# Kernel optimization log

Hardware: AMD Instinct MI355X
Metric: run time of the kernel (lower is better)

The kernel has to match this reference:

```python
import jax, jax.numpy as jnp
import numpy as np

B, S = 256, 512
NQ = 1000           # n_skills
MEM, DK, DV, FC = 20, 50, 200, 50  # memory_size, key dim, value dim, final fc dim


def _kaiming(key, shape, fan_in):
    return jax.random.normal(key, shape) * np.float32(np.sqrt(2.0 / fan_in))


def setup_inputs() -> dict:
    key = jax.random.key(0)
    ks = jax.random.split(key, 12)
    q_data = jax.random.randint(ks[0], (B, S), 0, NQ + 1)
    qa_data = jax.random.randint(ks[1], (B, S), 0, 2 * NQ + 1)
    u = jax.random.uniform(ks[2], (B * S,))
    # target: -1 = masked/padding, else binary label (matches target.ge(0) masking)
    target = jnp.where(u < 0.1, -1.0, (u > 0.55).astype(jnp.float32))
    q_embed_w = _kaiming(ks[3], (NQ + 1, DK), DK)
    qa_embed_w = _kaiming(ks[4], (2 * NQ + 1, DV), DV)
    memory_key = _kaiming(ks[5], (MEM, DK), DK)
    init_memory_value = _kaiming(ks[6], (MEM, DV), DV)
    erase_w = _kaiming(ks[7], (DV, DV), DV)
    erase_b = jnp.zeros((DV,), jnp.float32)
    add_w = _kaiming(ks[8], (DV, DV), DV)
    add_b = jnp.zeros((DV,), jnp.float32)
    read_w = _kaiming(ks[9], (DV + FC, FC), DV + FC)
    read_b = jnp.zeros((FC,), jnp.float32)
    pred_w = _kaiming(ks[10], (FC, 1), FC)
    pred_b = jnp.zeros((1,), jnp.float32)
    return dict(q_data=q_data, qa_data=qa_data, target=target,
                q_embed_w=q_embed_w, qa_embed_w=qa_embed_w,
                memory_key=memory_key, init_memory_value=init_memory_value,
                erase_w=erase_w, erase_b=erase_b, add_w=add_w, add_b=add_b,
                read_w=read_w, read_b=read_b, pred_w=pred_w, pred_b=pred_b)


def reference(q_data, qa_data, target, q_embed_w, qa_embed_w, memory_key,
              init_memory_value, erase_w, erase_b, add_w, add_b,
              read_w, read_b, pred_w, pred_b):
    b = q_data.shape[0]
    q_e = q_embed_w[q_data]     # [B,S,DK]
    qa_e = qa_embed_w[qa_data]  # [B,S,DV]
    Mv0 = jnp.broadcast_to(init_memory_value, (b, MEM, DV))

    def step(Mv, xs):
        q_t, qa_t = xs                                        # [B,DK], [B,DV]
        corr = jax.nn.softmax(q_t @ memory_key.T, axis=1)     # [B,MEM] addressing
        read = jnp.einsum('bm,bmd->bd', corr, Mv)             # weighted read
        erase = jax.nn.sigmoid(qa_t @ erase_w + erase_b)      # [B,DV]
        add = jnp.tanh(qa_t @ add_w + add_b)                  # [B,DV]
        w = corr[:, :, None]                                  # [B,MEM,1]
        Mv = Mv * (1.0 - w * erase[:, None, :]) + w * add[:, None, :]
        return Mv, read

    _, reads = jax.lax.scan(step, Mv0, (q_e.transpose(1, 0, 2), qa_e.transpose(1, 0, 2)))
    reads = reads.transpose(1, 0, 2)                          # [B,S,DV]
    x = jnp.concatenate([reads, q_e], axis=-1)                # [B,S,DV+FC]
    h = jnp.tanh(x @ read_w + read_b)                         # [B,S,FC]
    logits = (h @ pred_w + pred_b).reshape(-1)                # [B*S]
    mask = target >= 0.0
    t = jnp.where(mask, target, 0.0)
    # numerically-stable BCE-with-logits, masked mean
    bce = jnp.maximum(logits, 0.0) - logits * t + jnp.log1p(jnp.exp(-jnp.abs(logits)))
    loss = jnp.sum(jnp.where(mask, bce, 0.0)) / jnp.maximum(mask.sum(), 1)
    return loss, jax.nn.sigmoid(logits)
```

## Files before the change

### kernel.cpp

```cpp
#include <hip/hip_runtime.h>
#include <math.h>

#define B_   256
#define S_   512
#define NQ_  1000
#define MEM_ 20
#define DK_  50
#define DV_  200
#define FC_  50
#define RPB  2
#define CHK  16
#define CLEN (S_/CHK)
#define NKS  7
#define XS_STRIDE 232
#define CORR_STRIDE 12
#define NB_EA    ((2*NQ_+1+RPB-1)/RPB)
#define NB_CORR  4
#define NB_WPACK 7
#define NB_HQ    251
#define PREP1_BLOCKS (NB_EA+NB_CORR)
#define MM_BLOCKS (B_*CHK)
#define SCANA_BLOCKS (B_*(CHK-1))
#define SCANA_TOTAL (SCANA_BLOCKS+NB_WPACK+NB_HQ)

typedef __attribute__((ext_vector_type(8))) short bf16x8_t;
typedef __attribute__((ext_vector_type(4))) float f32x4_t;
typedef __attribute__((ext_vector_type(2))) _Float16 f16x2_t;

static __device__ __forceinline__ f16x2_t h2(unsigned u){ return __builtin_bit_cast(f16x2_t, u); }
static __device__ __forceinline__ unsigned h2u(f16x2_t v){ return __builtin_bit_cast(unsigned, v); }
static __device__ __forceinline__ unsigned packh2(float x, float y){
  unsigned short bx = __builtin_bit_cast(unsigned short, (_Float16)x);
  unsigned short by = __builtin_bit_cast(unsigned short, (_Float16)y);
  return (unsigned)bx | ((unsigned)by << 16);
}
static __device__ __forceinline__ f16x2_t pkfma16(f16x2_t a, f16x2_t b, f16x2_t c){
  return __builtin_elementwise_fma(a, b, c);
}
static __device__ __forceinline__ f16x2_t splat_l(f16x2_t p){ return __builtin_shufflevector(p, p, 0, 0); }
static __device__ __forceinline__ f16x2_t splat_h(f16x2_t p){ return __builtin_shufflevector(p, p, 1, 1); }

static __device__ __forceinline__ unsigned short f2bf(float f){
  unsigned u = __float_as_uint(f);
  unsigned r = u + 0x7fffu + ((u >> 16) & 1u);
  return (unsigned short)(r >> 16);
}
static __device__ __forceinline__ float ftanh(float x){
  float e = __expf(2.f*x);
  return 1.f - 2.f*__builtin_amdgcn_rcpf(e+1.f);
}
static __device__ __forceinline__ float fsigm(float x){
  return __builtin_amdgcn_rcpf(1.f+__expf(-x));
}

__global__ __launch_bounds__(256) void k_prep1(
    const float* __restrict__ qaw,
    const float* __restrict__ ew, const float* __restrict__ eb,
    const float* __restrict__ aw, const float* __restrict__ ab,
    unsigned* __restrict__ eaTab,
    const float* __restrict__ qw, const float* __restrict__ mk,
    unsigned* __restrict__ corrH){
  __shared__ float qa[RPB*DV_];
  int blk = blockIdx.x;
  if(blk < NB_EA){
    int row0 = blk*RPB;
    for(int i=threadIdx.x; i<RPB*DV_; i+=256){
      int r = i/DV_, cc = i - r*DV_;
      int row = row0 + r;
      qa[i] = (row <= 2*NQ_) ? qaw[row*DV_+cc] : 0.f;
    }
    __syncthreads();
    int d = threadIdx.x;
    if(d >= DV_) return;
    float accE[RPB], accA[RPB];
    #pragma unroll
    for(int r=0;r<RPB;++r){ accE[r] = eb[d]; accA[r] = ab[d]; }
    float we0 = ew[d], wa0 = aw[d];
    for(int j=0;j<DV_;++j){
      int jn = (j+1 < DV_) ? j+1 : j;
      float we1 = ew[jn*DV_+d];
      float wa1 = aw[jn*DV_+d];
      #pragma unroll
      for(int r=0;r<RPB;++r){
        float x = qa[r*DV_+j];
        accE[r] = fmaf(x, we0, accE[r]);
        accA[r] = fmaf(x, wa0, accA[r]);
      }
      we0 = we1; wa0 = wa1;
    }
    #pragma unroll
    for(int r=0;r<RPB;++r){
      int row = row0 + r;
      if(row <= 2*NQ_){
        unsigned he = (unsigned)__builtin_bit_cast(unsigned short, (_Float16)fsigm(accE[r]));
        unsigned ha = (unsigned)__builtin_bit_cast(unsigned short, (_Float16)ftanh(accA[r]));
        eaTab[(size_t)row*DV_+d] = he | (ha << 16);
      }
    }
  } else {
    int q = (blk-NB_EA)*256 + threadIdx.x;
    if(q > NQ_) return;
    float qv[DK_];
    #pragma unroll
    for(int j=0;j<DK_;++j) qv[j] = qw[q*DK_+j];
    float s[MEM_]; float mx = -1e30f;
    #pragma unroll
    for(int m=0;m<MEM_;++m){
      float acc = 0.f;
      #pragma unroll
      for(int j=0;j<DK_;++j) acc = fmaf(qv[j], mk[m*DK_+j], acc);
      s[m] = acc; mx = fmaxf(mx, acc);
    }
    float sum = 0.f;
    #pragma unroll
    for(int m=0;m<MEM_;++m){ s[m] = __expf(s[m]-mx); sum += s[m]; }
    float inv = __builtin_amdgcn_rcpf(sum);
    #pragma unroll
    for(int i=0;i<MEM_/2;++i)
      corrH[q*CORR_STRIDE+i] = packh2(s[2*i]*inv, s[2*i+1]*inv);
  }
}

#define STAGE_CHUNK(QP_G, QAP_G) { \
  int td = threadIdx.x; \
  if(td < CLEN){ \
    eaOffL[td] = (unsigned)(QAP_G)[td] * (DV_*4u); \
  } else if(td >= 64 && td < 64+160){ \
    int k = td - 64; \
    int t_ = (k*13108) >> 16;    \
    int j_ = k - t_*5; \
    int row_ = (QP_G)[t_]; \
    *(uint2*)&crL[t_*12 + j_*2] = \
      *(const uint2*)(corrH + (size_t)row_*CORR_STRIDE + j_*2); \
  } }

__global__ __launch_bounds__(256,8) void k_scanA(const int* __restrict__ qd,
    const int* __restrict__ qad,
    const unsigned* __restrict__ corrH,
    const unsigned* __restrict__ eaTab,
    unsigned* __restrict__ ABu,
    const float* __restrict__ qw,
    const float* __restrict__ rw, const float* __restrict__ rb,
    const float* __restrict__ pw,
    unsigned short* __restrict__ WpFrag, float* __restrict__ pwPad,
    float* __restrict__ hq){
  __shared__ __align__(16) unsigned crL[CLEN*12];
  __shared__ unsigned eaOffL[CLEN];
  const int blk = blockIdx.x;
  if(blk >= SCANA_BLOCKS){
    int xblk = blk - SCANA_BLOCKS;
    if(xblk < NB_WPACK){
      int ks = xblk;
      int nt = threadIdx.x >> 6;
      int lane = threadIdx.x & 63;
      int quad = lane >> 4, col = lane & 15;
      int n = nt*16 + col;
      unsigned short tmp[8];
      #pragma unroll
      for(int j=0;j<8;++j){
        int k = ks*32 + quad*8 + j;
        tmp[j] = (k < DV_ && n < FC_) ? f2bf(rw[k*FC_+n]) : (unsigned short)0;
      }
      uint4* dst = reinterpret_cast<uint4*>(WpFrag + ((size_t)(ks*4+nt)*64 + lane)*8);
      *dst = *reinterpret_cast<const uint4*>(tmp);
      if(ks == 0 && threadIdx.x < 64)
        pwPad[threadIdx.x] = (threadIdx.x < FC_) ? pw[threadIdx.x] : 0.f;
    } else {
      int idx = (xblk-NB_WPACK)*256 + threadIdx.x;
      int q = idx >> 6, n = idx & 63;
      if(q > NQ_) return;
      float v = 0.f;
      if(n < FC_){
        float acc = rb[n];
        #pragma unroll
        for(int j=0;j<DK_;++j)
          acc = fmaf(qw[q*DK_+j], rw[(DV_+j)*FC_+n], acc);
        v = acc;
      }
      hq[q*64+n] = v;
    }
    return;
  }

  const int b = blk / (CHK-1), c = blk % (CHK-1);
  const int d = threadIdx.x;
  const int dc = (d < DV_) ? d : DV_-1;
  const bool act = (d < DV_);
  const int* __restrict__ qp  = qd  + b*S_ + c*CLEN;
  const int* __restrict__ qap = qad + b*S_ + c*CLEN;

  STAGE_CHUNK(qp, qap)

  const f16x2_t one2h = {(_Float16)1.f, (_Float16)1.f};
  f16x2_t A2[MEM_/2], B2[MEM_/2];
  #pragma unroll
  for(int i=0;i<MEM_/2;++i){ A2[i] = one2h; B2[i] = (f16x2_t){(_Float16)0.f,(_Float16)0.f}; }

  __syncthreads();

  const char* eaB = (const char*)eaTab;
  const unsigned dcB = (unsigned)dc*4u;
  unsigned ea0 = *(const unsigned*)(eaB + eaOffL[0] + dcB);
  unsigned ea1 = *(const unsigned*)(eaB + eaOffL[1] + dcB);
  unsigned ea2 = *(const unsigned*)(eaB + eaOffL[2] + dcB);
  unsigned off3 = eaOffL[3], off4 = eaOffL[4], off5 = eaOffL[5];
  uint4 ca0 = *(const uint4*)&crL[0];  uint4 cb0 = *(const uint4*)&crL[4];  uint2 cc0 = *(const uint2*)&crL[8];
  uint4 ca1 = *(const uint4*)&crL[12]; uint4 cb1 = *(const uint4*)&crL[16]; uint2 cc1 = *(const uint2*)&crL[20];

  #pragma unroll 4
  for(int t=0;t<CLEN;++t){
    int t2 = (t+2 < CLEN) ? t+2 : CLEN-1;
    uint4 ca2 = *(const uint4*)&crL[t2*12];
    uint4 cb2 = *(const uint4*)&crL[t2*12+4];
    uint2 cc2 = *(const uint2*)&crL[t2*12+8];
    unsigned eanew = *(const unsigned*)(eaB + off3 + dcB);
    int t6 = (t+6 < CLEN) ? t+6 : CLEN-1;
    unsigned offnew = eaOffL[t6];

    f16x2_t pe = h2(ea0);
    const f16x2_t ee = splat_l(pe), aa = splat_h(pe);
    #define UPDA(u, i) { \
      f16x2_t cp = h2(u); \
      f16x2_t al = pkfma16(-cp, ee, one2h); \
      f16x2_t be = cp*aa; \
      A2[i] = A2[i]*al; \
      B2[i] = pkfma16(al, B2[i], be); }
    UPDA(ca0.x, 0)  UPDA(ca0.y, 1)  UPDA(ca0.z, 2)  UPDA(ca0.w, 3)
    UPDA(cb0.x, 4)  UPDA(cb0.y, 5)  UPDA(cb0.z, 6)  UPDA(cb0.w, 7)
    UPDA(cc0.x, 8)  UPDA(cc0.y, 9)
    #undef UPDA

    ca0=ca1; cb0=cb1; cc0=cc1;
    ca1=ca2; cb1=cb2; cc1=cc2;
    ea0=ea1; ea1=ea2; ea2=eanew;
    off3=off4; off4=off5; off5=offnew;
  }
  if(act){
    unsigned* base = ABu + ((size_t)(b*(CHK-1) + c)*MEM_)*DV_ + d;
    #pragma unroll
    for(int i=0;i<MEM_/2;++i){
      unsigned a01 = h2u(A2[i]);
      unsigned b01 = h2u(B2[i]);
      base[(size_t)(2*i)*DV_]   = (a01 & 0xffffu) | (b01 << 16);
      base[(size_t)(2*i+1)*DV_] = (a01 >> 16)     | (b01 & 0xffff0000u);
    }
  }
}

__global__ __launch_bounds__(256) void k_prefix(const float* __restrict__ mv0,
    const unsigned* __restrict__ ABu, unsigned* __restrict__ Mv0p){
  int i = blockIdx.x*256 + threadIdx.x;
  if(i >= B_*(MEM_/2)*DV_) return;
  int d = i % DV_;
  int p = (i / DV_) % (MEM_/2);
  int b = i / (DV_*(MEM_/2));
  float MvE = mv0[(2*p)*DV_+d];
  float MvO = mv0[(2*p+1)*DV_+d];
  #pragma unroll
  for(int c=1;c<CHK;++c){
    unsigned vE = ABu[((size_t)(b*(CHK-1) + (c-1))*MEM_ + 2*p)*DV_ + d];
    unsigned vO = ABu[((size_t)(b*(CHK-1) + (c-1))*MEM_ + 2*p+1)*DV_ + d];
    MvE = fmaf((float)h2(vE)[0], MvE, (float)h2(vE)[1]);
    MvO = fmaf((float)h2(vO)[0], MvO, (float)h2(vO)[1]);
    Mv0p[((size_t)(b*CHK + c)*(MEM_/2) + p)*DV_ + d] = packh2(MvE, MvO);
  }
}

__global__ __launch_bounds__(256,8) void k_scan_mm(const int* __restrict__ qd,
    const int* __restrict__ qad,
    const unsigned* __restrict__ corrH,
    const unsigned* __restrict__ eaTab,
    const float* __restrict__ mv0,
    const unsigned* __restrict__ Mv0p,
    const unsigned short* __restrict__ WpFrag,
    const float* __restrict__ hq,
    const float* __restrict__ pwPad, const float* __restrict__ pb,
    const float* __restrict__ target,
    float* __restrict__ out, float2* __restrict__ partials){
  __shared__ unsigned short Xs[CLEN*XS_STRIDE];
  __shared__ __align__(16) unsigned crL[CLEN*12];
  __shared__ unsigned eaOffL[CLEN];
  __shared__ float sred[2][2][16];
  __shared__ float sbce[4];

  const int blk = blockIdx.x;
  const int b = blk >> 4, c = blk & (CHK-1);
  const int d = threadIdx.x;
  const int dc = (d < DV_) ? d : DV_-1;
  const bool act = (d < DV_);
  const bool padw = (d < 224);
  const int* __restrict__ qp  = qd  + b*S_ + c*CLEN;
  const int* __restrict__ qap = qad + b*S_ + c*CLEN;

  const int wave = threadIdx.x >> 6;
  const int lane = threadIdx.x & 63;
  const int col  = lane & 15, quad = lane >> 4;
  const int rt   = wave & 1;
  const int nh   = wave >> 1;
  const int mbase = rt*16;

  STAGE_CHUNK(qp, qap)

  int qpre[4];
  #pragma unroll
  for(int reg=0;reg<4;++reg) qpre[reg] = qp[mbase + quad*4 + reg];

  f16x2_t Mv2[MEM_/2];
  if(c == 0){
    #pragma unroll
    for(int i=0;i<MEM_/2;++i)
      Mv2[i] = (f16x2_t){ (_Float16)mv0[(2*i)*DV_+dc], (_Float16)mv0[(2*i+1)*DV_+dc] };
  } else {
    const unsigned* base = Mv0p + ((size_t)(b*CHK + c)*(MEM_/2))*DV_ + dc;
    #pragma unroll
    for(int i=0;i<MEM_/2;++i)
      Mv2[i] = h2(base[(size_t)i*DV_]);
  }

  __syncthreads();

  const char* eaB = (const char*)eaTab;
  const unsigned dcB = (unsigned)dc*4u;
  unsigned ea0 = *(const unsigned*)(eaB + eaOffL[0] + dcB);
  unsigned ea1 = *(const unsigned*)(eaB + eaOffL[1] + dcB);
  unsigned ea2 = *(const unsigned*)(eaB + eaOffL[2] + dcB);
  unsigned off3 = eaOffL[3], off4 = eaOffL[4], off5 = eaOffL[5];
  uint4 ca0 = *(const uint4*)&crL[0];  uint4 cb0 = *(const uint4*)&crL[4];  uint2 cc0 = *(const uint2*)&crL[8];
  uint4 ca1 = *(const uint4*)&crL[12]; uint4 cb1 = *(const uint4*)&crL[16]; uint2 cc1 = *(const uint2*)&crL[20];

  #pragma unroll 4
  for(int t=0;t<CLEN;++t){
    int t2 = (t+2 < CLEN) ? t+2 : CLEN-1;
    uint4 ca2 = *(const uint4*)&crL[t2*12];
    uint4 cb2 = *(const uint4*)&crL[t2*12+4];
    uint2 cc2 = *(const uint2*)&crL[t2*12+8];
    unsigned eanew = *(const unsigned*)(eaB + off3 + dcB);
    int t6 = (t+6 < CLEN) ? t+6 : CLEN-1;
    unsigned offnew = eaOffL[t6];

    f16x2_t pe = h2(ea0);
    const f16x2_t ee = splat_l(pe), aa = splat_h(pe);
    float rd0 = 0.f, rd1 = 0.f;
    #define UPD2(u, i, acc) { \
      f16x2_t cp = h2(u); \
      acc = __builtin_amdgcn_fdot2(cp, Mv2[i], acc, false); \
      f16x2_t tt = pkfma16(-Mv2[i], ee, aa); \
      Mv2[i] = pkfma16(cp, tt, Mv2[i]); }
    UPD2(ca0.x, 0, rd0)  UPD2(ca0.y, 1, rd1)  UPD2(ca0.z, 2, rd0)  UPD2(ca0.w, 3, rd1)
    UPD2(cb0.x, 4, rd0)  UPD2(cb0.y, 5, rd1)  UPD2(cb0.z, 6, rd0)  UPD2(cb0.w, 7, rd1)
    UPD2(cc0.x, 8, rd0)  UPD2(cc0.y, 9, rd1)
    #undef UPD2

    if(padw) Xs[t*XS_STRIDE + d] = act ? f2bf(rd0+rd1) : (unsigned short)0;

    ca0=ca1; cb0=cb1; cc0=cc1;
    ca1=ca2; cb1=cb2; cc1=cc2;
    ea0=ea1; ea1=ea2; ea2=eanew;
    off3=off4; off4=off5; off5=offnew;
  }
  __syncthreads();

  float hqv[4][2];
  #pragma unroll
  for(int reg=0;reg<4;++reg)
    #pragma unroll
    for(int j=0;j<2;++j)
      hqv[reg][j] = hq[qpre[reg]*64 + (nh*2+j)*16 + col];

  f32x4_t acc[2];
  acc[0] = (f32x4_t){0.f,0.f,0.f,0.f};
  acc[1] = (f32x4_t){0.f,0.f,0.f,0.f};

  #pragma unroll
  for(int ks=0;ks<NKS;++ks){
    bf16x8_t a = *reinterpret_cast<const bf16x8_t*>(Xs + (mbase+col)*XS_STRIDE + quad*8 + ks*32);
    #pragma unroll
    for(int j=0;j<2;++j){
      int nt = nh*2 + j;
      bf16x8_t bfr = *reinterpret_cast<const bf16x8_t*>(WpFrag + ((size_t)(ks*4+nt)*64 + lane)*8);
      acc[j] = __builtin_amdgcn_mfma_f32_16x16x32_bf16(a, bfr, acc[j], 0, 0, 0);
    }
  }

  float part[4];
  #pragma unroll
  for(int reg=0;reg<4;++reg){
    float s = 0.f;
    #pragma unroll
    for(int j=0;j<2;++j){
      int n = (nh*2+j)*16 + col;
      float h = acc[j][reg] + hqv[reg][j];
      s = fmaf(pwPad[n], ftanh(h), s);
    }
    part[reg] = s;
  }
  #pragma unroll
  for(int off=1; off<16; off<<=1){
    #pragma unroll
    for(int reg=0;reg<4;++reg) part[reg] += __shfl_xor(part[reg], off, 64);
  }
  if(col == 0){
    #pragma unroll
    for(int reg=0;reg<4;++reg) sred[rt][nh][quad*4+reg] = part[reg];
  }
  __syncthreads();

  float bce = 0.f, cnt = 0.f;
  if(nh == 0 && col == 0){
    float pbv = pb[0];
    #pragma unroll
    for(int reg=0;reg<4;++reg){
      int idx = quad*4 + reg;
      int mloc = mbase + idx;
      int row = b*S_ + c*CLEN + mloc;
      float logit = sred[rt][0][idx] + sred[rt][1][idx] + pbv;
      out[1+row] = fsigm(logit);
      float t = target[row];
      if(t >= 0.f){
        cnt += 1.f;
        bce += fmaxf(logit,0.f) - logit*t + log1pf(__expf(-fabsf(logit)));
      }
    }
  }
  bce += __shfl_xor(bce, 16, 64); cnt += __shfl_xor(cnt, 16, 64);
  bce += __shfl_xor(bce, 32, 64); cnt += __shfl_xor(cnt, 32, 64);
  if(lane == 0 && nh == 0){ sbce[wave] = bce; sbce[2+wave] = cnt; }
  __syncthreads();
  if(threadIdx.x == 0)
    partials[blk] = make_float2(sbce[0]+sbce[1], sbce[2]+sbce[3]);
}

__global__ __launch_bounds__(256) void k_fin(const float2* __restrict__ partials,
                                             float* __restrict__ out){
  float bce = 0.f, cnt = 0.f;
  for(int i=threadIdx.x; i<MM_BLOCKS; i+=256){
    float2 p = partials[i];
    bce += p.x; cnt += p.y;
  }
  #pragma unroll
  for(int off=32; off>0; off>>=1){
    bce += __shfl_down(bce, off, 64);
    cnt += __shfl_down(cnt, off, 64);
  }
  __shared__ float sb[4], sc[4];
  int w = threadIdx.x >> 6;
  if((threadIdx.x & 63) == 0){ sb[w] = bce; sc[w] = cnt; }
  __syncthreads();
  if(threadIdx.x == 0){
    float Bt = sb[0]+sb[1]+sb[2]+sb[3];
    float Ct = sc[0]+sc[1]+sc[2]+sc[3];
    out[0] = Bt / fmaxf(Ct, 1.f);
  }
}

extern "C" void kernel_launch(void* const* d_in, const int* in_sizes, int n_in,
                              void* d_out, int out_size, void* d_ws, size_t ws_size,
                              hipStream_t stream){
  const int*   qd     = (const int*)d_in[0];
  const int*   qad    = (const int*)d_in[1];
  const float* target = (const float*)d_in[2];
  const float* qw     = (const float*)d_in[3];
  const float* qaw    = (const float*)d_in[4];
  const float* mk     = (const float*)d_in[5];
  const float* mv0    = (const float*)d_in[6];
  const float* ew     = (const float*)d_in[7];
  const float* eb     = (const float*)d_in[8];
  const float* aw     = (const float*)d_in[9];
  const float* ab     = (const float*)d_in[10];
  const float* rw     = (const float*)d_in[11];
  const float* rb     = (const float*)d_in[12];
  const float* pw     = (const float*)d_in[13];
  const float* pb     = (const float*)d_in[14];
  float* out = (float*)d_out;

  char* ws = (char*)d_ws;
  size_t off = 0;
  float2* partials = (float2*)(ws + off);            off += (size_t)MM_BLOCKS*8;
  unsigned* corrH = (unsigned*)(ws + off);           off += (((size_t)(NQ_+1)*CORR_STRIDE*4 + 255)/256)*256;
  unsigned* eaTab = (unsigned*)(ws + off);           off += (((size_t)(2*NQ_+1)*DV_*4 + 255)/256)*256;
  unsigned* ABu   = (unsigned*)(ws + off);           off += (size_t)SCANA_BLOCKS*MEM_*DV_*4;
  unsigned* Mv0p  = (unsigned*)(ws + off);           off += (size_t)MM_BLOCKS*(MEM_/2)*DV_*4;
  unsigned short* WpFrag = (unsigned short*)(ws + off); off += ((size_t)NKS*4*64*8*2 + 255)/256*256;
  float* pwPad    = (float*)(ws + off);              off += 256;
  float* hq       = (float*)(ws + off);              off += (size_t)(NQ_+1)*64*4;

  k_prep1<<<dim3(PREP1_BLOCKS), dim3(256), 0, stream>>>(qaw, ew, eb, aw, ab, eaTab,
                                                        qw, mk, corrH);
  k_scanA<<<dim3(SCANA_TOTAL), dim3(256), 0, stream>>>(qd, qad, corrH, eaTab,
                                                       ABu, qw, rw, rb, pw, WpFrag, pwPad, hq);
  k_prefix<<<dim3((B_*(MEM_/2)*DV_+255)/256), dim3(256), 0, stream>>>(mv0, ABu, Mv0p);
  k_scan_mm<<<dim3(MM_BLOCKS), dim3(256), 0, stream>>>(qd, qad, corrH, eaTab,
                                                       mv0, Mv0p, WpFrag, hq, pwPad, pb, target, out, partials);
  k_fin<<<dim3(1), dim3(256), 0, stream>>>(partials, out);
}
```

Baseline: 227.6 us.

## Process two batch rows per block in scan kernels to interleave independent recurrences

Each scanA and scan_mm block now handles two batch sequences, interleaving their per-step recurrence updates so the two independent dependency chains can hide each other's latency. Block count halves, launch bounds drop to 4 waves per SIMD, and the shared staging buffers are doubled. The aim is more instruction-level parallelism in the latency-bound sequential scan, at the cost of higher register use, lower occupancy and fewer blocks to spread across the GPU.

```diff
diff --git a/kernel.cpp b/kernel.cpp
--- a/kernel.cpp
+++ b/kernel.cpp
@@ -19,8 +19,9 @@
 #define NB_WPACK 7
 #define NB_HQ    251
 #define PREP1_BLOCKS (NB_EA+NB_CORR)
-#define MM_BLOCKS (B_*CHK)
-#define SCANA_BLOCKS (B_*(CHK-1))
+#define PAIRS (B_/2)
+#define MM_BLOCKS (PAIRS*CHK)
+#define SCANA_BLOCKS (PAIRS*(CHK-1))
 #define SCANA_TOTAL (SCANA_BLOCKS+NB_WPACK+NB_HQ)
 
 typedef __attribute__((ext_vector_type(8))) short bf16x8_t;
@@ -121,20 +122,22 @@
   }
 }
 
-#define STAGE_CHUNK(QP_G, QAP_G) { \
+#define STAGE2(QP0, QAP0, QP1, QAP1) { \
   int td = threadIdx.x; \
   if(td < CLEN){ \
-    eaOffL[td] = (unsigned)(QAP_G)[td] * (DV_*4u); \
-  } else if(td >= 64 && td < 64+160){ \
+    eaOffL[0][td] = (unsigned)(QAP0)[td] * (DV_*4u); \
+  } else if(td < 2*CLEN){ \
+    eaOffL[1][td-CLEN] = (unsigned)(QAP1)[td-CLEN] * (DV_*4u); \
+  } else if(td >= 64 && td < 224){ \
     int k = td - 64; \
     int t_ = (k*13108) >> 16;    \
     int j_ = k - t_*5; \
-    int row_ = (QP_G)[t_]; \
-    *(uint2*)&crL[t_*12 + j_*2] = \
-      *(const uint2*)(corrH + (size_t)row_*CORR_STRIDE + j_*2); \
+    int r0_ = (QP0)[t_], r1_ = (QP1)[t_]; \
+    *(uint2*)&crL[0][t_*12 + j_*2] = *(const uint2*)(corrH + (size_t)r0_*CORR_STRIDE + j_*2); \
+    *(uint2*)&crL[1][t_*12 + j_*2] = *(const uint2*)(corrH + (size_t)r1_*CORR_STRIDE + j_*2); \
   } }
 
-__global__ __launch_bounds__(256,8) void k_scanA(const int* __restrict__ qd,
+__global__ __launch_bounds__(256,4) void k_scanA(const int* __restrict__ qd,
     const int* __restrict__ qad,
     const unsigned* __restrict__ corrH,
     const unsigned* __restrict__ eaTab,
@@ -144,8 +147,8 @@
     const float* __restrict__ pw,
     unsigned short* __restrict__ WpFrag, float* __restrict__ pwPad,
     float* __restrict__ hq){
-  __shared__ __align__(16) unsigned crL[CLEN*12];
-  __shared__ unsigned eaOffL[CLEN];
+  __shared__ __align__(16) unsigned crL[2][CLEN*12];
+  __shared__ unsigned eaOffL[2][CLEN];
   const int blk = blockIdx.x;
   if(blk >= SCANA_BLOCKS){
     int xblk = blk - SCANA_BLOCKS;
@@ -182,67 +185,94 @@
     return;
   }
 
-  const int b = blk / (CHK-1), c = blk % (CHK-1);
+  const int pr = blk / (CHK-1), c = blk % (CHK-1);
+  const int b0 = 2*pr, b1 = 2*pr+1;
   const int d = threadIdx.x;
   const int dc = (d < DV_) ? d : DV_-1;
   const bool act = (d < DV_);
-  const int* __restrict__ qp  = qd  + b*S_ + c*CLEN;
-  const int* __restrict__ qap = qad + b*S_ + c*CLEN;
-
-  STAGE_CHUNK(qp, qap)
+  const int* __restrict__ qp0  = qd  + b0*S_ + c*CLEN;
+  const int* __restrict__ qap0 = qad + b0*S_ + c*CLEN;
+  const int* __restrict__ qp1  = qd  + b1*S_ + c*CLEN;
+  const int* __restrict__ qap1 = qad + b1*S_ + c*CLEN;
+
+  STAGE2(qp0, qap0, qp1, qap1)
 
   const f16x2_t one2h = {(_Float16)1.f, (_Float16)1.f};
-  f16x2_t A2[MEM_/2], B2[MEM_/2];
+  f16x2_t A2_0[MEM_/2], B2_0[MEM_/2], A2_1[MEM_/2], B2_1[MEM_/2];
   #pragma unroll
-  for(int i=0;i<MEM_/2;++i){ A2[i] = one2h; B2[i] = (f16x2_t){(_Float16)0.f,(_Float16)0.f}; }
-
+  for(int i=0;i<MEM_/2;++i){
+    A2_0[i] = one2h; B2_0[i] = (f16x2_t){(_Float16)0.f,(_Float16)0.f};
+    A2_1[i] = one2h; B2_1[i] = (f16x2_t){(_Float16)0.f,(_Float16)0.f};
+  }
   __syncthreads();
 
   const char* eaB = (const char*)eaTab;
   const unsigned dcB = (unsigned)dc*4u;
-  unsigned ea0 = *(const unsigned*)(eaB + eaOffL[0] + dcB);
-  unsigned ea1 = *(const unsigned*)(eaB + eaOffL[1] + dcB);
-  unsigned ea2 = *(const unsigned*)(eaB + eaOffL[2] + dcB);
-  unsigned off3 = eaOffL[3], off4 = eaOffL[4], off5 = eaOffL[5];
-  uint4 ca0 = *(const uint4*)&crL[0];  uint4 cb0 = *(const uint4*)&crL[4];  uint2 cc0 = *(const uint2*)&crL[8];
-  uint4 ca1 = *(const uint4*)&crL[12]; uint4 cb1 = *(const uint4*)&crL[16]; uint2 cc1 = *(const uint2*)&crL[20];
-
-  #pragma unroll 4
-  for(int t=0;t<CLEN;++t){
-    int t2 = (t+2 < CLEN) ? t+2 : CLEN-1;
-    uint4 ca2 = *(const uint4*)&crL[t2*12];
-    uint4 cb2 = *(const uint4*)&crL[t2*12+4];
-    uint2 cc2 = *(const uint2*)&crL[t2*12+8];
-    unsigned eanew = *(const unsigned*)(eaB + off3 + dcB);
-    int t6 = (t+6 < CLEN) ? t+6 : CLEN-1;
-    unsigned offnew = eaOffL[t6];
-
-    f16x2_t pe = h2(ea0);
-    const f16x2_t ee = splat_l(pe), aa = splat_h(pe);
-    #define UPDA(u, i) { \
-      f16x2_t cp = h2(u); \
-      f16x2_t al = pkfma16(-cp, ee, one2h); \
-      f16x2_t be = cp*aa; \
-      A2[i] = A2[i]*al; \
-      B2[i] = pkfma16(al, B2[i], be); }
-    UPDA(ca0.x, 0)  UPDA(ca0.y, 1)  UPDA(ca0.z, 2)  UPDA(ca0.w, 3)
-    UPDA(cb0.x, 4)  UPDA(cb0.y, 5)  UPDA(cb0.z, 6)  UPDA(cb0.w, 7)
-    UPDA(cc0.x, 8)  UPDA(cc0.y, 9)
-    #undef UPDA
-
-    ca0=ca1; cb0=cb1; cc0=cc1;
-    ca1=ca2; cb1=cb2; cc1=cc2;
-    ea0=ea1; ea1=ea2; ea2=eanew;
-    off3=off4; off4=off5; off5=offnew;
-  }
+  unsigned ea0A = *(const unsigned*)(eaB + eaOffL[0][0] + dcB);
+  unsigned ea0B = *(const unsigned*)(eaB + eaOffL[0][1] + dcB);
+  unsigned ea1A = *(const unsigned*)(eaB + eaOffL[1][0] + dcB);
+  unsigned ea1B = *(const unsigned*)(eaB + eaOffL[1][1] + dcB);
+  unsigned off0A = eaOffL[0][2], off0B = eaOffL[0][3];
+  unsigned off1A = eaOffL[1][2], off1B = eaOffL[1][3];
+  uint4 caA0 = *(const uint4*)&crL[0][0];  uint4 cbA0 = *(const uint4*)&crL[0][4];  uint2 ccA0 = *(const uint2*)&crL[0][8];
+  uint4 caB0 = *(const uint4*)&crL[0][12]; uint4 cbB0 = *(const uint4*)&crL[0][16]; uint2 ccB0 = *(const uint2*)&crL[0][20];
+  uint4 caA1 = *(const uint4*)&crL[1][0];  uint4 cbA1 = *(const uint4*)&crL[1][4];  uint2 ccA1 = *(const uint2*)&crL[1][8];
+  uint4 caB1 = *(const uint4*)&crL[1][12]; uint4 cbB1 = *(const uint4*)&crL[1][16]; uint2 ccB1 = *(const uint2*)&crL[1][20];
+
+  #define UPDA(u, i, AA, BB) { \
+    f16x2_t cp = h2(u); \
+    f16x2_t al = pkfma16(-cp, ee, one2h); \
+    f16x2_t be = cp*aa; \
+    AA[i] = AA[i]*al; \
+    BB[i] = pkfma16(al, BB[i], be); }
+  #define STEPA(EAU, CA, CB, CC, AA, BB) { \
+    f16x2_t pe = h2(EAU); \
+    const f16x2_t ee = splat_l(pe), aa = splat_h(pe); \
+    UPDA(CA.x, 0, AA, BB)  UPDA(CA.y, 1, AA, BB)  UPDA(CA.z, 2, AA, BB)  UPDA(CA.w, 3, AA, BB) \
+    UPDA(CB.x, 4, AA, BB)  UPDA(CB.y, 5, AA, BB)  UPDA(CB.z, 6, AA, BB)  UPDA(CB.w, 7, AA, BB) \
+    UPDA(CC.x, 8, AA, BB)  UPDA(CC.y, 9, AA, BB) }
+
+  #pragma unroll 1
+  for(int t=0;t<CLEN;t+=2){
+    STEPA(ea0A, caA0, cbA0, ccA0, A2_0, B2_0)
+    STEPA(ea1A, caA1, cbA1, ccA1, A2_1, B2_1)
+    {
+      int t2 = t+2; if(t2>CLEN-1) t2=CLEN-1;
+      caA0 = *(const uint4*)&crL[0][t2*12]; cbA0 = *(const uint4*)&crL[0][t2*12+4]; ccA0 = *(const uint2*)&crL[0][t2*12+8];
+      caA1 = *(const uint4*)&crL[1][t2*12]; cbA1 = *(const uint4*)&crL[1][t2*12+4]; ccA1 = *(const uint2*)&crL[1][t2*12+8];
+      ea0A = *(const unsigned*)(eaB + off0A + dcB);
+      ea1A = *(const unsigned*)(eaB + off1A + dcB);
+      int t4 = t+4; if(t4>CLEN-1) t4=CLEN-1;
+      off0A = eaOffL[0][t4]; off1A = eaOffL[1][t4];
+    }
+    STEPA(ea0B, caB0, cbB0, ccB0, A2_0, B2_0)
+    STEPA(ea1B, caB1, cbB1, ccB1, A2_1, B2_1)
+    {
+      int t3 = t+3; if(t3>CLEN-1) t3=CLEN-1;
+      caB0 = *(const uint4*)&crL[0][t3*12]; cbB0 = *(const uint4*)&crL[0][t3*12+4]; ccB0 = *(const uint2*)&crL[0][t3*12+8];
+      caB1 = *(const uint4*)&crL[1][t3*12]; cbB1 = *(const uint4*)&crL[1][t3*12+4]; ccB1 = *(const uint2*)&crL[1][t3*12+8];
+      ea0B = *(const unsigned*)(eaB + off0B + dcB);
+      ea1B = *(const unsigned*)(eaB + off1B + dcB);
+      int t5 = t+5; if(t5>CLEN-1) t5=CLEN-1;
+      off0B = eaOffL[0][t5]; off1B = eaOffL[1][t5];
+    }
+  }
+  #undef STEPA
+  #undef UPDA
+
   if(act){
-    unsigned* base = ABu + ((size_t)(b*(CHK-1) + c)*MEM_)*DV_ + d;
+    unsigned* base0 = ABu + ((size_t)(b0*(CHK-1) + c)*MEM_)*DV_ + d;
+    unsigned* base1 = ABu + ((size_t)(b1*(CHK-1) + c)*MEM_)*DV_ + d;
     #pragma unroll
     for(int i=0;i<MEM_/2;++i){
-      unsigned a01 = h2u(A2[i]);
-      unsigned b01 = h2u(B2[i]);
-      base[(size_t)(2*i)*DV_]   = (a01 & 0xffffu) | (b01 << 16);
-      base[(size_t)(2*i+1)*DV_] = (a01 >> 16)     | (b01 & 0xffff0000u);
+      unsigned a01 = h2u(A2_0[i]);
+      unsigned b01 = h2u(B2_0[i]);
+      base0[(size_t)(2*i)*DV_]   = (a01 & 0xffffu) | (b01 << 16);
+      base0[(size_t)(2*i+1)*DV_] = (a01 >> 16)     | (b01 & 0xffff0000u);
+      unsigned a11 = h2u(A2_1[i]);
+      unsigned b11 = h2u(B2_1[i]);
+      base1[(size_t)(2*i)*DV_]   = (a11 & 0xffffu) | (b11 << 16);
+      base1[(size_t)(2*i+1)*DV_] = (a11 >> 16)     | (b11 & 0xffff0000u);
     }
   }
 }
@@ -266,7 +296,7 @@
   }
 }
 
-__global__ __launch_bounds__(256,8) void k_scan_mm(const int* __restrict__ qd,
+__global__ __launch_bounds__(256,4) void k_scan_mm(const int* __restrict__ qd,
     const int* __restrict__ qad,
     const unsigned* __restrict__ corrH,
     const unsigned* __restrict__ eaTab,
@@ -277,20 +307,23 @@
     const float* __restrict__ pwPad, const float* __restrict__ pb,
     const float* __restrict__ target,
     float* __restrict__ out, float2* __restrict__ partials){
-  __shared__ unsigned short Xs[CLEN*XS_STRIDE];
-  __shared__ __align__(16) unsigned crL[CLEN*12];
-  __shared__ unsigned eaOffL[CLEN];
+  __shared__ unsigned short Xs[2][CLEN*XS_STRIDE];
+  __shared__ __align__(16) unsigned crL[2][CLEN*12];
+  __shared__ unsigned eaOffL[2][CLEN];
   __shared__ float sred[2][2][16];
   __shared__ float sbce[4];
 
   const int blk = blockIdx.x;
-  const int b = blk >> 4, c = blk & (CHK-1);
+  const int pr = blk >> 4, c = blk & (CHK-1);
+  const int b0 = 2*pr, b1 = 2*pr+1;
   const int d = threadIdx.x;
   const int dc = (d < DV_) ? d : DV_-1;
   const bool act = (d < DV_);
   const bool padw = (d < 224);
-  const int* __restrict__ qp  = qd  + b*S_ + c*CLEN;
-  const int* __restrict__ qap = qad + b*S_ + c*CLEN;
+  const int* __restrict__ qp0  = qd  + b0*S_ + c*CLEN;
+  const int* __restrict__ qap0 = qad + b0*S_ + c*CLEN;
+  const int* __restrict__ qp1  = qd  + b1*S_ + c*CLEN;
+  const int* __restrict__ qap1 = qad + b1*S_ + c*CLEN;
 
   const int wave = threadIdx.x >> 6;
   const int lane = threadIdx.x & 63;
@@ -299,132 +332,162 @@
   const int nh   = wave >> 1;
   const int mbase = rt*16;
 
-  STAGE_CHUNK(qp, qap)
-
-  int qpre[4];
+  STAGE2(qp0, qap0, qp1, qap1)
+
+  int qpre0[4], qpre1[4];
   #pragma unroll
-  for(int reg=0;reg<4;++reg) qpre[reg] = qp[mbase + quad*4 + reg];
-
-  f16x2_t Mv2[MEM_/2];
+  for(int reg=0;reg<4;++reg){
+    qpre0[reg] = qp0[mbase + quad*4 + reg];
+    qpre1[reg] = qp1[mbase + quad*4 + reg];
+  }
+
+  f16x2_t Mv0_[MEM_/2], Mv1_[MEM_/2];
   if(c == 0){
     #pragma unroll
-    for(int i=0;i<MEM_/2;++i)
-      Mv2[i] = (f16x2_t){ (_Float16)mv0[(2*i)*DV_+dc], (_Float16)mv0[(2*i+1)*DV_+dc] };
+    for(int i=0;i<MEM_/2;++i){
+      f16x2_t v = { (_Float16)mv0[(2*i)*DV_+dc], (_Float16)mv0[(2*i+1)*DV_+dc] };
+      Mv0_[i] = v; Mv1_[i] = v;
+    }
   } else {
-    const unsigned* base = Mv0p + ((size_t)(b*CHK + c)*(MEM_/2))*DV_ + dc;
-    #pragma unroll
-    for(int i=0;i<MEM_/2;++i)
-      Mv2[i] = h2(base[(size_t)i*DV_]);
-  }
-
+    const unsigned* base0 = Mv0p + ((size_t)(b0*CHK + c)*(MEM_/2))*DV_ + dc;
+    const unsigned* base1 = Mv0p + ((size_t)(b1*CHK + c)*(MEM_/2))*DV_ + dc;
+    #pragma unroll
+    for(int i=0;i<MEM_/2;++i){
+      Mv0_[i] = h2(base0[(size_t)i*DV_]);
+      Mv1_[i] = h2(base1[(size_t)i*DV_]);
+    }
+  }
   __syncthreads();
 
   const char* eaB = (const char*)eaTab;
   const unsigned dcB = (unsigned)dc*4u;
-  unsigned ea0 = *(const unsigned*)(eaB + eaOffL[0] + dcB);
-  unsigned ea1 = *(const unsigned*)(eaB + eaOffL[1] + dcB);
-  unsigned ea2 = *(const unsigned*)(eaB + eaOffL[2] + dcB);
-  unsigned off3 = eaOffL[3], off4 = eaOffL[4], off5 = eaOffL[5];
-  uint4 ca0 = *(const uint4*)&crL[0];  uint4 cb0 = *(const uint4*)&crL[4];  uint2 cc0 = *(const uint2*)&crL[8];
-  uint4 ca1 = *(const uint4*)&crL[12]; uint4 cb1 = *(const uint4*)&crL[16]; uint2 cc1 = *(const uint2*)&crL[20];
-
-  #pragma unroll 4
-  for(int t=0;t<CLEN;++t){
-    int t2 = (t+2 < CLEN) ? t+2 : CLEN-1;
-    uint4 ca2 = *(const uint4*)&crL[t2*12];
-    uint4 cb2 = *(const uint4*)&crL[t2*12+4];
-    uint2 cc2 = *(const uint2*)&crL[t2*12+8];
-    unsigned eanew = *(const unsigned*)(eaB + off3 + dcB);
-    int t6 = (t+6 < CLEN) ? t+6 : CLEN-1;
-    unsigned offnew = eaOffL[t6];
-
-    f16x2_t pe = h2(ea0);
-    const f16x2_t ee = splat_l(pe), aa = splat_h(pe);
-    float rd0 = 0.f, rd1 = 0.f;
-    #define UPD2(u, i, acc) { \
-      f16x2_t cp = h2(u); \
-      acc = __builtin_amdgcn_fdot2(cp, Mv2[i], acc, false); \
-      f16x2_t tt = pkfma16(-Mv2[i], ee, aa); \
-      Mv2[i] = pkfma16(cp, tt, Mv2[i]); }
-    UPD2(ca0.x, 0, rd0)  UPD2(ca0.y, 1, rd1)  UPD2(ca0.z, 2, rd0)  UPD2(ca0.w, 3, rd1)
-    UPD2(cb0.x, 4, rd0)  UPD2(cb0.y, 5, rd1)  UPD2(cb0.z, 6, rd0)  UPD2(cb0.w, 7, rd1)
-    UPD2(cc0.x, 8, rd0)  UPD2(cc0.y, 9, rd1)
-    #undef UPD2
-
-    if(padw) Xs[t*XS_STRIDE + d] = act ? f2bf(rd0+rd1) : (unsigned short)0;
-
-    ca0=ca1; cb0=cb1; cc0=cc1;
-    ca1=ca2; cb1=cb2; cc1=cc2;
-    ea0=ea1; ea1=ea2; ea2=eanew;
-    off3=off4; off4=off5; off5=offnew;
-  }
+  unsigned ea0A = *(const unsigned*)(eaB + eaOffL[0][0] + dcB);
+  unsigned ea0B = *(const unsigned*)(eaB + eaOffL[0][1] + dcB);
+  unsigned ea1A = *(const unsigned*)(eaB + eaOffL[1][0] + dcB);
+  unsigned ea1B = *(const unsigned*)(eaB + eaOffL[1][1] + dcB);
+  unsigned off0A = eaOffL[0][2], off0B = eaOffL[0][3];
+  unsigned off1A = eaOffL[1][2], off1B = eaOffL[1][3];
+  uint4 caA0 = *(const uint4*)&crL[0][0];  uint4 cbA0 = *(const uint4*)&crL[0][4];  uint2 ccA0 = *(const uint2*)&crL[0][8];
+  uint4 caB0 = *(const uint4*)&crL[0][12]; uint4 cbB0 = *(const uint4*)&crL[0][16]; uint2 ccB0 = *(const uint2*)&crL[0][20];
+  uint4 caA1 = *(const uint4*)&crL[1][0];  uint4 cbA1 = *(const uint4*)&crL[1][4];  uint2 ccA1 = *(const uint2*)&crL[1][8];
+  uint4 caB1 = *(const uint4*)&crL[1][12]; uint4 cbB1 = *(const uint4*)&crL[1][16]; uint2 ccB1 = *(const uint2*)&crL[1][20];
+
+  #define UPD2(u, i, acc, MV) { \
+    f16x2_t cp = h2(u); \
+    acc = __builtin_amdgcn_fdot2(cp, MV[i], acc, false); \
+    f16x2_t tt = pkfma16(-MV[i], ee, aa); \
+    MV[i] = pkfma16(cp, tt, MV[i]); }
+  #define STEPMM(S, T_, EAU, CA, CB, CC, MV) { \
+    f16x2_t pe = h2(EAU); \
+    const f16x2_t ee = splat_l(pe), aa = splat_h(pe); \
+    float rd0 = 0.f, rd1 = 0.f; \
+    UPD2(CA.x, 0, rd0, MV)  UPD2(CA.y, 1, rd1, MV)  UPD2(CA.z, 2, rd0, MV)  UPD2(CA.w, 3, rd1, MV) \
+    UPD2(CB.x, 4, rd0, MV)  UPD2(CB.y, 5, rd1, MV)  UPD2(CB.z, 6, rd0, MV)  UPD2(CB.w, 7, rd1, MV) \
+    UPD2(CC.x, 8, rd0, MV)  UPD2(CC.y, 9, rd1, MV) \
+    if(padw) Xs[S][(T_)*XS_STRIDE + d] = act ? f2bf(rd0+rd1) : (unsigned short)0; }
+
+  #pragma unroll 1
+  for(int t=0;t<CLEN;t+=2){
+    STEPMM(0, t, ea0A, caA0, cbA0, ccA0, Mv0_)
+    STEPMM(1, t, ea1A, caA1, cbA1, ccA1, Mv1_)
+    {
+      int t2 = t+2; if(t2>CLEN-1) t2=CLEN-1;
+      caA0 = *(const uint4*)&crL[0][t2*12]; cbA0 = *(const uint4*)&crL[0][t2*12+4]; ccA0 = *(const uint2*)&crL[0][t2*12+8];
+      caA1 = *(const uint4*)&crL[1][t2*12]; cbA1 = *(const uint4*)&crL[1][t2*12+4]; ccA1 = *(const uint2*)&crL[1][t2*12+8];
+      ea0A = *(const unsigned*)(eaB + off0A + dcB);
+      ea1A = *(const unsigned*)(eaB + off1A + dcB);
+      int t4 = t+4; if(t4>CLEN-1) t4=CLEN-1;
+      off0A = eaOffL[0][t4]; off1A = eaOffL[1][t4];
+    }
+    STEPMM(0, t+1, ea0B, caB0, cbB0, ccB0, Mv0_)
+    STEPMM(1, t+1, ea1B, caB1, cbB1, ccB1, Mv1_)
+    {
+      int t3 = t+3; if(t3>CLEN-1) t3=CLEN-1;
+      caB0 = *(const uint4*)&crL[0][t3*12]; cbB0 = *(const uint4*)&crL[0][t3*12+4]; ccB0 = *(const uint2*)&crL[0][t3*12+8];
+      caB1 = *(const uint4*)&crL[1][t3*12]; cbB1 = *(const uint4*)&crL[1][t3*12+4]; ccB1 = *(const uint2*)&crL[1][t3*12+8];
+      ea0B = *(const unsigned*)(eaB + off0B + dcB);
+      ea1B = *(const unsigned*)(eaB + off1B + dcB);
+      int t5 = t+5; if(t5>CLEN-1) t5=CLEN-1;
+      off0B = eaOffL[0][t5]; off1B = eaOffL[1][t5];
+    }
+  }
+  #undef STEPMM
+  #undef UPD2
   __syncthreads();
 
-  float hqv[4][2];
+  float hqv0[4][2], hqv1[4][2];
   #pragma unroll
   for(int reg=0;reg<4;++reg)
     #pragma unroll
-    for(int j=0;j<2;++j)
-      hqv[reg][j] = hq[qpre[reg]*64 + (nh*2+j)*16 + col];
-
-  f32x4_t acc[2];
-  acc[0] = (f32x4_t){0.f,0.f,0.f,0.f};
-  acc[1] = (f32x4_t){0.f,0.f,0.f,0.f};
-
-  #pragma unroll
-  for(int ks=0;ks<NKS;++ks){
-    bf16x8_t a = *reinterpret_cast<const bf16x8_t*>(Xs + (mbase+col)*XS_STRIDE + quad*8 + ks*32);
-    #pragma unroll
     for(int j=0;j<2;++j){
-      int nt = nh*2 + j;
-      bf16x8_t bfr = *reinterpret_cast<const bf16x8_t*>(WpFrag + ((size_t)(ks*4+nt)*64 + lane)*8);
-      acc[j] = __builtin_amdgcn_mfma_f32_16x16x32_bf16(a, bfr, acc[j], 0, 0, 0);
-    }
-  }
-
-  float part[4];
-  #pragma unroll
-  for(int reg=0;reg<4;++reg){
-    float s = 0.f;
-    #pragma unroll
-    for(int j=0;j<2;++j){
-      int n = (nh*2+j)*16 + col;
-      float h = acc[j][reg] + hqv[reg][j];
-      s = fmaf(pwPad[n], ftanh(h), s);
-    }
-    part[reg] = s;
-  }
-  #pragma unroll
-  for(int off=1; off<16; off<<=1){
-    #pragma unroll
-    for(int reg=0;reg<4;++reg) part[reg] += __shfl_xor(part[reg], off, 64);
-  }
-  if(col == 0){
-    #pragma unroll
-    for(int reg=0;reg<4;++reg) sred[rt][nh][quad*4+reg] = part[reg];
-  }
-  __syncthreads();
-
-  float bce = 0.f, cnt = 0.f;
-  if(nh == 0 && col == 0){
-    float pbv = pb[0];
+      hqv0[reg][j] = hq[qpre0[reg]*64 + (nh*2+j)*16 + col];
+      hqv1[reg][j] = hq[qpre1[reg]*64 + (nh*2+j)*16 + col];
+    }
+
+  float bceAcc = 0.f, cntAcc = 0.f;
+  const float pbv = pb[0];
+
+  #pragma unroll 1
+  for(int s=0;s<2;++s){
+    f32x4_t acc[2];
+    acc[0] = (f32x4_t){0.f,0.f,0.f,0.f};
+    acc[1] = (f32x4_t){0.f,0.f,0.f,0.f};
+    #pragma unroll
+    for(int ks=0;ks<NKS;++ks){
+      bf16x8_t a = *reinterpret_cast<const bf16x8_t*>(Xs[s] + (mbase+col)*XS_STRIDE + quad*8 + ks*32);
+      #pragma unroll
+      for(int j=0;j<2;++j){
+        int nt = nh*2 + j;
+        bf16x8_t bfr = *reinterpret_cast<const bf16x8_t*>(WpFrag + ((size_t)(ks*4+nt)*64 + lane)*8);
+        acc[j] = __builtin_amdgcn_mfma_f32_16x16x32_bf16(a, bfr, acc[j], 0, 0, 0);
+      }
+    }
+
+    float part[4];
     #pragma unroll
     for(int reg=0;reg<4;++reg){
-      int idx = quad*4 + reg;
-      int mloc = mbase + idx;
-      int row = b*S_ + c*CLEN + mloc;
-      float logit = sred[rt][0][idx] + sred[rt][1][idx] + pbv;
-      out[1+row] = fsigm(logit);
-      float t = target[row];
-      if(t >= 0.f){
-        cnt += 1.f;
-        bce += fmaxf(logit,0.f) - logit*t + log1pf(__expf(-fabsf(logit)));
-      }
-    }
-  }
-  bce += __shfl_xor(bce, 16, 64); cnt += __shfl_xor(cnt, 16, 64);
-  bce += __shfl_xor(bce, 32, 64); cnt += __shfl_xor(cnt, 32, 64);
-  if(lane == 0 && nh == 0){ sbce[wave] = bce; sbce[2+wave] = cnt; }
+      float sAcc = 0.f;
+      #pragma unroll
+      for(int j=0;j<2;++j){
+        int n = (nh*2+j)*16 + col;
+        float h = acc[j][reg] + (s==0 ? hqv0[reg][j] : hqv1[reg][j]);
+        sAcc = fmaf(pwPad[n], ftanh(h), sAcc);
+      }
+      part[reg] = sAcc;
+    }
+    #pragma unroll
+    for(int off=1; off<16; off<<=1){
+      #pragma unroll
+      for(int reg=0;reg<4;++reg) part[reg] += __shfl_xor(part[reg], off, 64);
+    }
+    if(col == 0){
+      #pragma unroll
+      for(int reg=0;reg<4;++reg) sred[rt][nh][quad*4+reg] = part[reg];
+    }
+    __syncthreads();
+
+    if(nh == 0 && col == 0){
+      int bs = (s==0) ? b0 : b1;
+      #pragma unroll
+      for(int reg=0;reg<4;++reg){
+        int idx = quad*4 + reg;
+        int mloc = mbase + idx;
+        int row = bs*S_ + c*CLEN + mloc;
+        float logit = sred[rt][0][idx] + sred[rt][1][idx] + pbv;
+        out[1+row] = fsigm(logit);
+        float t = target[row];
+        if(t >= 0.f){
+          cntAcc += 1.f;
+          bceAcc += fmaxf(logit,0.f) - logit*t + log1pf(__expf(-fabsf(logit)));
+        }
+      }
+    }
+    __syncthreads();
+  }
+
+  bceAcc += __shfl_xor(bceAcc, 16, 64); cntAcc += __shfl_xor(cntAcc, 16, 64);
+  bceAcc += __shfl_xor(bceAcc, 32, 64); cntAcc += __shfl_xor(cntAcc, 32, 64);
+  if(lane == 0 && nh == 0){ sbce[wave] = bceAcc; sbce[2+wave] = cntAcc; }
   __syncthreads();
   if(threadIdx.x == 0)
     partials[blk] = make_float2(sbce[0]+sbce[1], sbce[2]+sbce[3]);
@@ -478,8 +541,8 @@
   float2* partials = (float2*)(ws + off);            off += (size_t)MM_BLOCKS*8;
   unsigned* corrH = (unsigned*)(ws + off);           off += (((size_t)(NQ_+1)*CORR_STRIDE*4 + 255)/256)*256;
   unsigned* eaTab = (unsigned*)(ws + off);           off += (((size_t)(2*NQ_+1)*DV_*4 + 255)/256)*256;
-  unsigned* ABu   = (unsigned*)(ws + off);           off += (size_t)SCANA_BLOCKS*MEM_*DV_*4;
-  unsigned* Mv0p  = (unsigned*)(ws + off);           off += (size_t)MM_BLOCKS*(MEM_/2)*DV_*4;
+  unsigned* ABu   = (unsigned*)(ws + off);           off += (size_t)B_*(CHK-1)*MEM_*DV_*4;
+  unsigned* Mv0p  = (unsigned*)(ws + off);           off += (size_t)B_*CHK*(MEM_/2)*DV_*4;
   unsigned short* WpFrag = (unsigned short*)(ws + off); off += ((size_t)NKS*4*64*8*2 + 255)/256*256;
   float* pwPad    = (float*)(ws + off);              off += 256;
   float* hq       = (float*)(ws + off);              off += (size_t)(NQ_+1)*64*4;
```

Measured after the change: 244.0 us. 7.2% more time.
